# Kernel tuning notes

Measured on AMD Instinct MI355X. Metric: run time of the kernel, lower is better.

## Reference

```python
import jax, jax.numpy as jnp
import numpy as np

B, T, C, H = 2, 2048, 2048, 16
HD = C // H  # 128 head dim
ROPE_BASE = 10000.0


def setup_inputs() -> dict:
    key = jax.random.key(0)
    k0, k1, k2 = jax.random.split(key, 3)
    x = jax.random.normal(k0, (B, T, C), dtype=jnp.float32)
    W_attn = jax.random.normal(k1, (C, 3 * C), dtype=jnp.float32) * 0.02
    b_attn = jnp.zeros((3 * C,), dtype=jnp.float32)
    W_proj = jax.random.normal(k2, (C, C), dtype=jnp.float32) * 0.02
    b_proj = jnp.zeros((C,), dtype=jnp.float32)
    # freqs_cis = exp(i * t * theta_j), represented as (cos, sin), shape [T, HD//2]
    inv_freq = 1.0 / (ROPE_BASE ** (jnp.arange(0, HD, 2, dtype=jnp.float32) / HD))
    freqs = jnp.outer(jnp.arange(T, dtype=jnp.float32), inv_freq)
    return {"x": x, "W_attn": W_attn, "b_attn": b_attn, "W_proj": W_proj,
            "b_proj": b_proj, "cos": jnp.cos(freqs), "sin": jnp.sin(freqs)}


def _apply_rope(v, cos, sin):
    # v: [B, T, H, HD]; pairs (v[..., 2i], v[..., 2i+1]) rotated by angle freqs[t, i]
    vr = v.reshape(v.shape[:-1] + (-1, 2))
    x0, x1 = vr[..., 0], vr[..., 1]
    c = cos[None, :, None, :]  # [1, T, 1, HD//2]
    s = sin[None, :, None, :]
    o0 = x0 * c - x1 * s
    o1 = x0 * s + x1 * c
    return jnp.stack([o0, o1], axis=-1).reshape(v.shape)


def reference(x, W_attn, b_attn, W_proj, b_proj, cos, sin):
    Bv, Tv, Cv = x.shape
    qkv = x @ W_attn + b_attn                      # [B, T, 3C]
    q, k, v = jnp.split(qkv, 3, axis=-1)
    q = q.reshape(Bv, Tv, H, HD)
    k = k.reshape(Bv, Tv, H, HD)
    v = v.reshape(Bv, Tv, H, HD)
    q = _apply_rope(q, cos, sin)
    k = _apply_rope(k, cos, sin)
    scale = 1.0 / jnp.sqrt(jnp.float32(HD))
    att = jnp.einsum('bqhd,bkhd->bhqk', q, k) * scale
    causal = jnp.tril(jnp.ones((Tv, Tv), dtype=bool))
    att = jnp.where(causal[None, None], att, jnp.finfo(att.dtype).min)
    att = jax.nn.softmax(att, axis=-1)
    y = jnp.einsum('bhqk,bkhd->bqhd', att, v).reshape(Bv, Tv, Cv)
    return y @ W_proj + b_proj
```

## Files before the change

### kernel.cpp

```cpp
#include <hip/hip_runtime.h>

typedef unsigned short u16;
typedef __attribute__((ext_vector_type(8))) short short8;
typedef __attribute__((ext_vector_type(4))) float f32x4;

#define TSEQ 2048
#define NHEAD 16
#define HDIM 128

__device__ __forceinline__ u16 f2bf(float x) {
    unsigned u = __float_as_uint(x);
    return (u16)((u + 0x7fffu + ((u >> 16) & 1u)) >> 16);
}
__device__ __forceinline__ float b2f(u16 h) {
    return __uint_as_float(((unsigned)h) << 16);
}
__device__ __forceinline__ void async16(const void* g, void* l) {
    __builtin_amdgcn_global_load_lds((__attribute__((address_space(1))) void*)(void*)g,
                                     (__attribute__((address_space(3))) void*)l, 16, 0, 0);
}
__device__ __forceinline__ f32x4 zero4() {
    f32x4 z = {0.f, 0.f, 0.f, 0.f};
    return z;
}

template <int CTRL>
__device__ __forceinline__ float dppf(float x) {
    return __int_as_float(__builtin_amdgcn_mov_dpp(__float_as_int(x), CTRL, 0xf, 0xf, true));
}
__device__ __forceinline__ float dpp_max16(float x) {
    x = fmaxf(x, dppf<0xB1>(x));
    x = fmaxf(x, dppf<0x4E>(x));
    x = fmaxf(x, dppf<0x141>(x));
    x = fmaxf(x, dppf<0x140>(x));
    return x;
}
__device__ __forceinline__ float dpp_sum16(float x) {
    x += dppf<0xB1>(x);
    x += dppf<0x4E>(x);
    x += dppf<0x141>(x);
    x += dppf<0x140>(x);
    return x;
}

__global__ void cast_bf16(const float4* __restrict__ in, ushort4* __restrict__ out, int n4) {
    int i = blockIdx.x * 256 + threadIdx.x;
    if (i < n4) {
        float4 v = in[i];
        ushort4 o;
        o.x = f2bf(v.x); o.y = f2bf(v.y); o.z = f2bf(v.z); o.w = f2bf(v.w);
        out[i] = o;
    }
}

__global__ void transpose_cast(const float* __restrict__ in, u16* __restrict__ out, int K, int N) {
    __shared__ float tile[64][65];
    int n0 = blockIdx.x * 64, k0 = blockIdx.y * 64;
    int tx = threadIdx.x & 63, ty = threadIdx.x >> 6;
#pragma unroll
    for (int i = 0; i < 16; i++) {
        int r = ty + i * 4;
        tile[r][tx] = in[(size_t)(k0 + r) * N + n0 + tx];
    }
    __syncthreads();
#pragma unroll
    for (int i = 0; i < 16; i++) {
        int r = ty + i * 4;
        out[(size_t)(n0 + r) * K + k0 + tx] = f2bf(tile[tx][r]);
    }
}

template <int MODE>
__global__ __launch_bounds__(256) void gemm_bt(
    const u16* __restrict__ A, const u16* __restrict__ Bt, const float* __restrict__ bias,
    float* __restrict__ outf, u16* __restrict__ qb, u16* __restrict__ kb, u16* __restrict__ vT,
    const float* __restrict__ cosp, const float* __restrict__ sinp,
    int M, int N, int K) {
    __shared__ __align__(16) u16 smem[8704];
    u16* As = smem;
    u16* Bs = smem + 4096;
    const int tid = threadIdx.x;
    const int wave = tid >> 6, lane = tid & 63;
    const int low = lane & 15, quad = lane >> 4;
    const int m0 = blockIdx.y * 128, n0 = blockIdx.x * 128;
    const int wm = (wave >> 1) * 64, wn = (wave & 1) * 64;
    const int ldr = lane >> 2;
    const int ldc = (lane & 3) * 8;

    f32x4 acc[4][4];
#pragma unroll
    for (int i = 0; i < 4; i++)
#pragma unroll
        for (int j = 0; j < 4; j++) acc[i][j] = zero4();

    for (int k0 = 0; k0 < K; k0 += 32) {
#pragma unroll
        for (int c = 0; c < 2; ++c) {
            const int chunk = wave * 2 + c;
            const int row = chunk * 16 + ldr;
            async16(A + (size_t)(m0 + row) * K + k0 + ldc, As + chunk * 512);
            async16(Bt + (size_t)(n0 + row) * K + k0 + ldc, Bs + chunk * 512);
        }
        __syncthreads();
        short8 af[4], bfv[4];
#pragma unroll
        for (int i = 0; i < 4; i++) af[i] = *(const short8*)(As + (wm + i * 16 + low) * 32 + quad * 8);
#pragma unroll
        for (int j = 0; j < 4; j++) bfv[j] = *(const short8*)(Bs + (wn + j * 16 + low) * 32 + quad * 8);
#pragma unroll
        for (int i = 0; i < 4; i++)
#pragma unroll
            for (int j = 0; j < 4; j++)
                acc[i][j] = __builtin_amdgcn_mfma_f32_16x16x32_bf16(af[i], bfv[j], acc[i][j], 0, 0, 0);
        __syncthreads();
    }

    if (MODE == 1) {
#pragma unroll
        for (int j = 0; j < 4; j++) {
            const int ng = n0 + wn + j * 16 + low;
            const float bv = bias[ng];
#pragma unroll
            for (int i = 0; i < 4; i++) {
                const int rbase = m0 + wm + i * 16 + quad * 4;
#pragma unroll
                for (int r = 0; r < 4; r++)
                    outf[(size_t)(rbase + r) * N + ng] = acc[i][j][r] + bv;
            }
        }
        return;
    }
}


#define WAIT_DS()                                          \
    {                                                      \
        asm volatile("s_waitcnt lgkmcnt(0)" ::: "memory"); \
        __builtin_amdgcn_sched_barrier(0);                 \
    }
#define PRIO_MFQ(MB, NB)                \
    {                                   \
        __builtin_amdgcn_s_setprio(1);  \
        MFQ(MB, NB);                    \
        __builtin_amdgcn_s_setprio(0);  \
    }
#define BAR() __builtin_amdgcn_s_barrier();
#define VBAR(N)                                                \
    {                                                          \
        asm volatile("s_waitcnt vmcnt(" #N ")" ::: "memory");  \
        __builtin_amdgcn_s_barrier();                          \
    }

#define STAGE(GP, GROW0, LB, KT)                                                                     \
    {                                                                                                \
        const int ktc__ = ((KT) < NT ? (KT) : NT - 1);                                               \
        const u16* g0__ = (GP) + (size_t)((GROW0) + wave * 16 + grow) * (size_t)K + ktc__ * 64 +     \
                          gslot * 8;                                                                 \
        u16* l0__ = (LB) + wave * 1024;                                                              \
        async16(g0__, l0__);                                                                         \
        async16(g0__ + (size_t)8 * K, l0__ + 512);                                                   \
    }

#define LDA4(BASE, MB)                                                              \
    {                                                                               \
        _Pragma("unroll") for (int mm = 0; mm < 4; ++mm) {                          \
            a[mm][0] = *(const short8*)((BASE) + aoff0 + ((MB) + mm) * 1024);       \
            a[mm][1] = *(const short8*)((BASE) + aoff1 + ((MB) + mm) * 1024);       \
        }                                                                           \
    }
#define LDB2(BASE, NB)                                                              \
    {                                                                               \
        _Pragma("unroll") for (int nn = 0; nn < 2; ++nn) {                          \
            b[(NB) + nn][0] = *(const short8*)((BASE) + boff0 + ((NB) + nn) * 1024);\
            b[(NB) + nn][1] = *(const short8*)((BASE) + boff1 + ((NB) + nn) * 1024);\
        }                                                                           \
    }
#define MFQ(MB, NB)                                                                                   \
    {                                                                                                 \
        _Pragma("unroll") for (int mm = 0; mm < 4; ++mm) _Pragma("unroll") for (int nn = 0; nn < 2;   \
                                                                                ++nn) {               \
            acc[(MB) + mm][(NB) + nn] = __builtin_amdgcn_mfma_f32_16x16x32_bf16(                      \
                a[mm][0], b[(NB) + nn][0], acc[(MB) + mm][(NB) + nn], 0, 0, 0);                       \
            acc[(MB) + mm][(NB) + nn] = __builtin_amdgcn_mfma_f32_16x16x32_bf16(                      \
                a[mm][1], b[(NB) + nn][1], acc[(MB) + mm][(NB) + nn], 0, 0, 0);                       \
        }                                                                                             \
    }

__global__ __launch_bounds__(512, 2) void gemm256(
    const u16* __restrict__ A, const u16* __restrict__ Bt, const float* __restrict__ bias,
    u16* __restrict__ qb, u16* __restrict__ kb, u16* __restrict__ vT,
    const float* __restrict__ cosp, const float* __restrict__ sinp,
    int M, int N, int K) {
    extern __shared__ u16 sm[];
    u16* const smA0 = sm;
    u16* const smB0 = sm + 16384;
    u16* const smA1 = sm + 32768;
    u16* const smB1 = sm + 49152;

    const int tid = threadIdx.x;
    const int wave = tid >> 6, lane = tid & 63;
    const int low = lane & 15, quad = lane >> 4;
    const int wr = wave >> 2, wc = wave & 3;
    const int m0 = blockIdx.y * 256, n0 = blockIdx.x * 256;
    const int NT = K >> 6;

    const int grow = lane >> 3;
    const int gslot = (lane & 7) ^ grow;

    const int swz = low & 7;
    const int arow = (wr * 128 + low) * 64;
    const int brow = (wc * 64 + low) * 64;
    const int aoff0 = arow + ((0 + quad) ^ swz) * 8;
    const int aoff1 = arow + ((4 + quad) ^ swz) * 8;
    const int boff0 = brow + ((0 + quad) ^ swz) * 8;
    const int boff1 = brow + ((4 + quad) ^ swz) * 8;

    f32x4 acc[8][4];
#pragma unroll
    for (int i = 0; i < 8; i++)
#pragma unroll
        for (int j = 0; j < 4; j++) acc[i][j] = zero4();
    short8 a[4][2], b[4][2];

    STAGE(A, m0, smA0, 0);
    STAGE(A, m0 + 128, smA0 + 8192, 0);
    STAGE(Bt, n0, smB0, 0);
    STAGE(Bt, n0 + 128, smB0 + 8192, 0);
    STAGE(A, m0, smA1, 1);
    STAGE(A, m0 + 128, smA1 + 8192, 1);
    STAGE(Bt, n0, smB1, 1);
    STAGE(Bt, n0 + 128, smB1 + 8192, 1);
    asm volatile("s_waitcnt vmcnt(8)" ::: "memory");
    __builtin_amdgcn_s_barrier();

#pragma unroll 1
    for (int it = 0; it < (NT >> 1); ++it) {
        const int e = it * 2;
        LDA4(smA0, 0);
        LDB2(smB0, 0);
        WAIT_DS(); PRIO_MFQ(0, 0);
        LDB2(smB0, 2);
        WAIT_DS(); PRIO_MFQ(0, 2);
        LDA4(smA0, 4);
        WAIT_DS();
        BAR();
        PRIO_MFQ(4, 2);
        STAGE(A, m0, smA0, e + 2);
        STAGE(Bt, n0, smB0, e + 2);
        PRIO_MFQ(4, 0);
        VBAR(4);
        LDA4(smA1, 0);
        LDB2(smB1, 0);
        STAGE(A, m0 + 128, smA0 + 8192, e + 2);
        STAGE(Bt, n0 + 128, smB0 + 8192, e + 2);
        WAIT_DS(); PRIO_MFQ(0, 0);
        LDB2(smB1, 2);
        WAIT_DS(); PRIO_MFQ(0, 2);
        LDA4(smA1, 4);
        WAIT_DS();
        BAR();
        PRIO_MFQ(4, 2);
        STAGE(A, m0, smA1, e + 3);
        STAGE(A, m0 + 128, smA1 + 8192, e + 3);
        STAGE(Bt, n0, smB1, e + 3);
        STAGE(Bt, n0 + 128, smB1 + 8192, e + 3);
        PRIO_MFQ(4, 0);
        VBAR(8);
    }

    asm volatile("s_waitcnt vmcnt(0)" ::: "memory");
    __syncthreads();

    const int which = n0 >> 11;
    const int h0 = (n0 & 2047) >> 7;
    const int bb = m0 >> 11, t0 = m0 & 2047;
    float bvv[4];
#pragma unroll
    for (int nn = 0; nn < 4; ++nn) bvv[nn] = bias[n0 + wc * 64 + nn * 16 + low];

    if (which < 2) {
        u16* dstb = (which == 0 ? qb : kb);
        u16* epi = sm;
#pragma unroll
        for (int hh = 0; hh < 2; ++hh) {
            if ((wc >> 1) == hh) {
#pragma unroll
                for (int mm = 0; mm < 8; ++mm)
#pragma unroll
                    for (int nn = 0; nn < 4; ++nn)
#pragma unroll
                        for (int rr = 0; rr < 4; ++rr)
                            epi[(wr * 128 + mm * 16 + quad * 4 + rr) * 136 +
                                (wc & 1) * 64 + nn * 16 + low] = f2bf(acc[mm][nn][rr] + bvv[nn]);
            }
            __syncthreads();
            {
                const int row = tid >> 1, dh = (tid & 1) * 64;
                const int t = t0 + row;
                u16* dr = dstb + (((size_t)(bb * NHEAD + h0 + hh)) * TSEQ + t) * HDIM + dh;
                u16 vals[64];
#pragma unroll
                for (int qq = 0; qq < 8; ++qq)
                    *(short8*)(vals + qq * 8) = *(const short8*)(epi + row * 136 + dh + qq * 8);
                float csv[32], snv[32];
#pragma unroll
                for (int qq = 0; qq < 8; ++qq) {
                    *(float4*)(csv + qq * 4) =
                        *(const float4*)(cosp + (size_t)t * 64 + (dh >> 1) + qq * 4);
                    *(float4*)(snv + qq * 4) =
                        *(const float4*)(sinp + (size_t)t * 64 + (dh >> 1) + qq * 4);
                }
                u16 ov[64];
#pragma unroll
                for (int pp = 0; pp < 32; ++pp) {
                    float x0 = b2f(vals[2 * pp]), x1 = b2f(vals[2 * pp + 1]);
                    ov[2 * pp] = f2bf(x0 * csv[pp] - x1 * snv[pp]);
                    ov[2 * pp + 1] = f2bf(x0 * snv[pp] + x1 * csv[pp]);
                }
#pragma unroll
                for (int qq = 0; qq < 8; ++qq)
                    *(short8*)(dr + qq * 8) = *(const short8*)(ov + qq * 8);
            }
            __syncthreads();
        }
    } else {
        u16* epi = sm;
#pragma unroll
        for (int hh = 0; hh < 2; ++hh) {
            if ((wc >> 1) == hh) {
#pragma unroll
                for (int mm = 0; mm < 8; ++mm)
#pragma unroll
                    for (int nn = 0; nn < 4; ++nn)
#pragma unroll
                        for (int rr = 0; rr < 4; ++rr)
                            epi[((wc & 1) * 64 + nn * 16 + low) * 264 +
                                wr * 128 + mm * 16 + quad * 4 + rr] = f2bf(acc[mm][nn][rr] + bvv[nn]);
            }
            __syncthreads();
            {
                const int dd = tid >> 2, tc = (tid & 3) * 64;
                u16* dr = vT + ((size_t)(bb * NHEAD + h0 + hh) * HDIM + dd) * TSEQ + t0 + tc;
#pragma unroll
                for (int qq = 0; qq < 8; ++qq)
                    *(short8*)(dr + qq * 8) = *(const short8*)(epi + dd * 264 + tc + qq * 8);
            }
            __syncthreads();
        }
    }
}

__global__ __launch_bounds__(256) void flash_attn(const u16* __restrict__ qb, const u16* __restrict__ kb,
                                                  const u16* __restrict__ vT, u16* __restrict__ y) {
    __shared__ u16 Ks[64 * 128];
    __shared__ u16 Vs[128 * 64];
    __shared__ u16 Ps[4][16 * 72];
    const int tid = threadIdx.x;
    const int wave = tid >> 6, lane = tid & 63;
    const int low = lane & 15, quad = lane >> 4;
    const int bh = blockIdx.x;
    const int qt = 31 - blockIdx.y;
    const int q0 = qt * 64 + wave * 16;
    const float scale2 = 0.08838834764831845f * 1.44269504088896f;

    const u16* Qp = qb + ((size_t)bh * TSEQ + q0) * HDIM;
    short8 qf[4];
#pragma unroll
    for (int c = 0; c < 4; c++) qf[c] = *(const short8*)(Qp + (size_t)low * HDIM + c * 32 + quad * 8);

    f32x4 o[8];
#pragma unroll
    for (int d = 0; d < 8; d++) o[d] = zero4();
    float m_i[4], l_i[4];
#pragma unroll
    for (int r = 0; r < 4; r++) { m_i[r] = -1e30f; l_i[r] = 0.f; }

    const u16* Kb = kb + (size_t)bh * TSEQ * HDIM;
    const u16* Vb = vT + (size_t)bh * HDIM * TSEQ;
    u16* Pw = &Ps[wave][0];
    const int ntiles = qt + 1;

    const int krow = tid >> 4, kchunk = tid & 15;
    const int vrow = tid >> 3, vchunk = tid & 7;

    for (int kt = 0; kt < ntiles; ++kt) {
        const int kv0 = kt * 64;
#pragma unroll
        for (int j = 0; j < 4; j++) {
            const int row = j * 16 + krow;
            const int gc = kchunk ^ (row & 7);
            async16(Kb + (size_t)(kv0 + row) * HDIM + gc * 8, Ks + row * 128 + kchunk * 8);
        }
#pragma unroll
        for (int j = 0; j < 4; j++) {
            const int d = j * 32 + vrow;
            const int gc = vchunk ^ (d & 7);
            async16(Vb + (size_t)d * TSEQ + kv0 + gc * 8, Vs + d * 64 + vchunk * 8);
        }
        __syncthreads();

        f32x4 s[4];
#pragma unroll
        for (int h = 0; h < 4; h++) s[h] = zero4();
#pragma unroll
        for (int h = 0; h < 4; h++) {
            const int row = h * 16 + low;
#pragma unroll
            for (int c = 0; c < 4; c++) {
                const int cc = c * 4 + quad;
                short8 kf = *(const short8*)(Ks + row * 128 + (cc ^ (row & 7)) * 8);
                s[h] = __builtin_amdgcn_mfma_f32_16x16x32_bf16(qf[c], kf, s[h], 0, 0, 0);
            }
        }

        float alpha[4];
#pragma unroll
        for (int r = 0; r < 4; r++) {
            const int qg = q0 + quad * 4 + r;
            float sv[4];
#pragma unroll
            for (int h = 0; h < 4; h++)
                sv[h] = (kv0 + h * 16 + low <= qg) ? s[h][r] * scale2 : -1e30f;
            float mx = fmaxf(fmaxf(sv[0], sv[1]), fmaxf(sv[2], sv[3]));
            mx = dpp_max16(mx);
            float mnew = fmaxf(m_i[r], mx);
            alpha[r] = exp2f(m_i[r] - mnew);
            m_i[r] = mnew;
            float p0 = exp2f(sv[0] - mnew);
            float p1 = exp2f(sv[1] - mnew);
            float p2 = exp2f(sv[2] - mnew);
            float p3 = exp2f(sv[3] - mnew);
            float rs = (p0 + p1) + (p2 + p3);
            rs = dpp_sum16(rs);
            l_i[r] = l_i[r] * alpha[r] + rs;
            const int prow = (quad * 4 + r) * 72;
            Pw[prow + low] = f2bf(p0);
            Pw[prow + 16 + low] = f2bf(p1);
            Pw[prow + 32 + low] = f2bf(p2);
            Pw[prow + 48 + low] = f2bf(p3);
        }
        __threadfence_block();

#pragma unroll
        for (int d = 0; d < 8; ++d)
#pragma unroll
            for (int r = 0; r < 4; r++) o[d][r] *= alpha[r];

#pragma unroll
        for (int kc = 0; kc < 2; kc++) {
            short8 pf = *(const short8*)(Pw + low * 72 + kc * 32 + quad * 8);
#pragma unroll
            for (int dd = 0; dd < 8; ++dd) {
                const int vr = dd * 16 + low;
                const int cc = kc * 4 + quad;
                short8 vf = *(const short8*)(Vs + vr * 64 + (cc ^ (vr & 7)) * 8);
                o[dd] = __builtin_amdgcn_mfma_f32_16x16x32_bf16(pf, vf, o[dd], 0, 0, 0);
            }
        }
        __syncthreads();
    }

    const int b = bh >> 4, h = bh & 15;
#pragma unroll
    for (int r = 0; r < 4; r++) {
        float inv = 1.0f / l_i[r];
        size_t row = (size_t)(b * TSEQ + q0 + quad * 4 + r);
        u16* yp = y + row * 2048 + h * HDIM;
#pragma unroll
        for (int d = 0; d < 8; ++d) yp[d * 16 + low] = f2bf(o[d][r] * inv);
    }
}

extern "C" void kernel_launch(void* const* d_in, const int* in_sizes, int n_in,
                              void* d_out, int out_size, void* d_ws, size_t ws_size,
                              hipStream_t stream) {
    const float* x = (const float*)d_in[0];
    const float* Wa = (const float*)d_in[1];
    const float* ba = (const float*)d_in[2];
    const float* Wp = (const float*)d_in[3];
    const float* bp = (const float*)d_in[4];
    const float* cs = (const float*)d_in[5];
    const float* sn = (const float*)d_in[6];
    float* out = (float*)d_out;

    u16* xb = (u16*)d_ws;
    u16* Wab = xb + 8388608;
    u16* Wpb = Wab + 12582912;
    u16* qb = Wpb + 4194304;
    u16* kb = qb + 8388608;
    u16* vT = kb + 8388608;
    u16* y = xb;

    static bool attr_set = false;
    if (!attr_set) {
        hipFuncSetAttribute(reinterpret_cast<const void*>(gemm256),
                            hipFuncAttributeMaxDynamicSharedMemorySize, 131072);
        attr_set = true;
    }

    cast_bf16<<<8192, 256, 0, stream>>>((const float4*)x, (ushort4*)xb, 2097152);
    transpose_cast<<<dim3(96, 32), 256, 0, stream>>>(Wa, Wab, 2048, 6144);
    transpose_cast<<<dim3(32, 32), 256, 0, stream>>>(Wp, Wpb, 2048, 2048);
    gemm256<<<dim3(24, 16), 512, 131072, stream>>>(xb, Wab, ba, qb, kb, vT, cs, sn, 4096, 6144, 2048);
    flash_attn<<<dim3(32, 32), 256, 0, stream>>>(qb, kb, vT, y);
    gemm_bt<1><<<dim3(16, 32), 256, 0, stream>>>(y, Wpb, bp, out, nullptr, nullptr, nullptr, nullptr, nullptr, 4096, 2048, 2048);
}
```

Before: 421.3 us.

## Replace output projection GEMM with pipelined 128x256 kernel and peel QKV loop tail

Replaces the simple single-buffered output-projection GEMM with a new double-buffered, swizzled-LDS, 512-thread 128x256-tile kernel that prefetches async loads ahead of MFMA work. The QKV GEMM main loop now runs one fewer iteration and peels the last two K-steps into an epilogue, which removes the clamped redundant prefetches. It also drops the intermediate LDS waits between the MFMA groups. The intent is to hide global-load latency and raise MFMA utilization in both GEMMs. The cost is more LDS per block and reliance on the compiler inserting correct waits where the explicit ones were removed.

```diff
diff --git a/kernel.cpp b/kernel.cpp
--- a/kernel.cpp
+++ b/kernel.cpp
@@ -70,95 +70,26 @@
     }
 }
 
-template <int MODE>
-__global__ __launch_bounds__(256) void gemm_bt(
-    const u16* __restrict__ A, const u16* __restrict__ Bt, const float* __restrict__ bias,
-    float* __restrict__ outf, u16* __restrict__ qb, u16* __restrict__ kb, u16* __restrict__ vT,
-    const float* __restrict__ cosp, const float* __restrict__ sinp,
-    int M, int N, int K) {
-    __shared__ __align__(16) u16 smem[8704];
-    u16* As = smem;
-    u16* Bs = smem + 4096;
-    const int tid = threadIdx.x;
-    const int wave = tid >> 6, lane = tid & 63;
-    const int low = lane & 15, quad = lane >> 4;
-    const int m0 = blockIdx.y * 128, n0 = blockIdx.x * 128;
-    const int wm = (wave >> 1) * 64, wn = (wave & 1) * 64;
-    const int ldr = lane >> 2;
-    const int ldc = (lane & 3) * 8;
-
-    f32x4 acc[4][4];
-#pragma unroll
-    for (int i = 0; i < 4; i++)
-#pragma unroll
-        for (int j = 0; j < 4; j++) acc[i][j] = zero4();
-
-    for (int k0 = 0; k0 < K; k0 += 32) {
-#pragma unroll
-        for (int c = 0; c < 2; ++c) {
-            const int chunk = wave * 2 + c;
-            const int row = chunk * 16 + ldr;
-            async16(A + (size_t)(m0 + row) * K + k0 + ldc, As + chunk * 512);
-            async16(Bt + (size_t)(n0 + row) * K + k0 + ldc, Bs + chunk * 512);
-        }
-        __syncthreads();
-        short8 af[4], bfv[4];
-#pragma unroll
-        for (int i = 0; i < 4; i++) af[i] = *(const short8*)(As + (wm + i * 16 + low) * 32 + quad * 8);
-#pragma unroll
-        for (int j = 0; j < 4; j++) bfv[j] = *(const short8*)(Bs + (wn + j * 16 + low) * 32 + quad * 8);
-#pragma unroll
-        for (int i = 0; i < 4; i++)
-#pragma unroll
-            for (int j = 0; j < 4; j++)
-                acc[i][j] = __builtin_amdgcn_mfma_f32_16x16x32_bf16(af[i], bfv[j], acc[i][j], 0, 0, 0);
-        __syncthreads();
-    }
-
-    if (MODE == 1) {
-#pragma unroll
-        for (int j = 0; j < 4; j++) {
-            const int ng = n0 + wn + j * 16 + low;
-            const float bv = bias[ng];
-#pragma unroll
-            for (int i = 0; i < 4; i++) {
-                const int rbase = m0 + wm + i * 16 + quad * 4;
-#pragma unroll
-                for (int r = 0; r < 4; r++)
-                    outf[(size_t)(rbase + r) * N + ng] = acc[i][j][r] + bv;
-            }
-        }
-        return;
-    }
-}
-
-
 #define WAIT_DS()                                          \
     {                                                      \
         asm volatile("s_waitcnt lgkmcnt(0)" ::: "memory"); \
         __builtin_amdgcn_sched_barrier(0);                 \
     }
-#define PRIO_MFQ(MB, NB)                \
-    {                                   \
-        __builtin_amdgcn_s_setprio(1);  \
-        MFQ(MB, NB);                    \
-        __builtin_amdgcn_s_setprio(0);  \
-    }
 #define BAR() __builtin_amdgcn_s_barrier();
-#define VBAR(N)                                                \
+#define VBAR_(N)                                               \
     {                                                          \
         asm volatile("s_waitcnt vmcnt(" #N ")" ::: "memory");  \
         __builtin_amdgcn_s_barrier();                          \
     }
-
-#define STAGE(GP, GROW0, LB, KT)                                                                     \
-    {                                                                                                \
-        const int ktc__ = ((KT) < NT ? (KT) : NT - 1);                                               \
-        const u16* g0__ = (GP) + (size_t)((GROW0) + wave * 16 + grow) * (size_t)K + ktc__ * 64 +     \
-                          gslot * 8;                                                                 \
-        u16* l0__ = (LB) + wave * 1024;                                                              \
-        async16(g0__, l0__);                                                                         \
-        async16(g0__ + (size_t)8 * K, l0__ + 512);                                                   \
+#define VBAR(N) VBAR_(N)
+
+#define STAGE(GP, GROW0, LB, KT)                                                                 \
+    {                                                                                            \
+        const u16* g0__ = (GP) + (size_t)((GROW0) + wave * 16 + grow) * (size_t)K + (KT)*64 +    \
+                          gslot * 8;                                                             \
+        u16* l0__ = (LB) + wave * 1024;                                                          \
+        async16(g0__, l0__);                                                                     \
+        async16(g0__ + (size_t)8 * K, l0__ + 512);                                               \
     }
 
 #define LDA4(BASE, MB)                                                              \
@@ -184,6 +115,12 @@
             acc[(MB) + mm][(NB) + nn] = __builtin_amdgcn_mfma_f32_16x16x32_bf16(                      \
                 a[mm][1], b[(NB) + nn][1], acc[(MB) + mm][(NB) + nn], 0, 0, 0);                       \
         }                                                                                             \
+    }
+#define PRIO_MFQ(MB, NB)                \
+    {                                   \
+        __builtin_amdgcn_s_setprio(1);  \
+        MFQ(MB, NB);                    \
+        __builtin_amdgcn_s_setprio(0);  \
     }
 
 __global__ __launch_bounds__(512, 2) void gemm256(
@@ -230,17 +167,17 @@
     STAGE(A, m0 + 128, smA1 + 8192, 1);
     STAGE(Bt, n0, smB1, 1);
     STAGE(Bt, n0 + 128, smB1 + 8192, 1);
-    asm volatile("s_waitcnt vmcnt(8)" ::: "memory");
-    __builtin_amdgcn_s_barrier();
-
+    VBAR(8);
+
+    const int NI = (NT >> 1) - 1;
 #pragma unroll 1
-    for (int it = 0; it < (NT >> 1); ++it) {
+    for (int it = 0; it < NI; ++it) {
         const int e = it * 2;
         LDA4(smA0, 0);
         LDB2(smB0, 0);
-        WAIT_DS(); PRIO_MFQ(0, 0);
         LDB2(smB0, 2);
-        WAIT_DS(); PRIO_MFQ(0, 2);
+        PRIO_MFQ(0, 0);
+        PRIO_MFQ(0, 2);
         LDA4(smA0, 4);
         WAIT_DS();
         BAR();
@@ -251,11 +188,11 @@
         VBAR(4);
         LDA4(smA1, 0);
         LDB2(smB1, 0);
+        LDB2(smB1, 2);
         STAGE(A, m0 + 128, smA0 + 8192, e + 2);
         STAGE(Bt, n0 + 128, smB0 + 8192, e + 2);
-        WAIT_DS(); PRIO_MFQ(0, 0);
-        LDB2(smB1, 2);
-        WAIT_DS(); PRIO_MFQ(0, 2);
+        PRIO_MFQ(0, 0);
+        PRIO_MFQ(0, 2);
         LDA4(smA1, 4);
         WAIT_DS();
         BAR();
@@ -267,8 +204,24 @@
         PRIO_MFQ(4, 0);
         VBAR(8);
     }
-
-    asm volatile("s_waitcnt vmcnt(0)" ::: "memory");
+    LDA4(smA0, 0);
+    LDB2(smB0, 0);
+    LDB2(smB0, 2);
+    PRIO_MFQ(0, 0);
+    PRIO_MFQ(0, 2);
+    LDA4(smA0, 4);
+    PRIO_MFQ(4, 2);
+    PRIO_MFQ(4, 0);
+    VBAR(0);
+    LDA4(smA1, 0);
+    LDB2(smB1, 0);
+    LDB2(smB1, 2);
+    PRIO_MFQ(0, 0);
+    PRIO_MFQ(0, 2);
+    LDA4(smA1, 4);
+    PRIO_MFQ(4, 2);
+    PRIO_MFQ(4, 0);
+
     __syncthreads();
 
     const int which = n0 >> 11;
@@ -346,6 +299,120 @@
                     *(short8*)(dr + qq * 8) = *(const short8*)(epi + dd * 264 + tc + qq * 8);
             }
             __syncthreads();
+        }
+    }
+}
+
+#define PMFQ(NB)                                                                                      \
+    {                                                                                                 \
+        _Pragma("unroll") for (int mm = 0; mm < 4; ++mm) _Pragma("unroll") for (int nn = 0; nn < 2;   \
+                                                                                ++nn) {               \
+            acc[mm][(NB) + nn] = __builtin_amdgcn_mfma_f32_16x16x32_bf16(                             \
+                a[mm][0], b[(NB) + nn][0], acc[mm][(NB) + nn], 0, 0, 0);                              \
+            acc[mm][(NB) + nn] = __builtin_amdgcn_mfma_f32_16x16x32_bf16(                             \
+                a[mm][1], b[(NB) + nn][1], acc[mm][(NB) + nn], 0, 0, 0);                              \
+        }                                                                                             \
+    }
+#define PPRIO_MFQ(NB)                   \
+    {                                   \
+        __builtin_amdgcn_s_setprio(1);  \
+        PMFQ(NB);                       \
+        __builtin_amdgcn_s_setprio(0);  \
+    }
+
+__global__ __launch_bounds__(512, 2) void pgemm(
+    const u16* __restrict__ A, const u16* __restrict__ Bt, const float* __restrict__ bias,
+    float* __restrict__ outf, int M, int N, int K) {
+    extern __shared__ u16 sm[];
+    u16* const smA0 = sm;
+    u16* const smB0 = sm + 8192;
+    u16* const smA1 = sm + 24576;
+    u16* const smB1 = sm + 32768;
+
+    const int tid = threadIdx.x;
+    const int wave = tid >> 6, lane = tid & 63;
+    const int low = lane & 15, quad = lane >> 4;
+    const int wr = wave >> 2, wc = wave & 3;
+    const int m0 = blockIdx.y * 128, n0 = blockIdx.x * 256;
+    const int NT = K >> 6;
+
+    const int grow = lane >> 3;
+    const int gslot = (lane & 7) ^ grow;
+
+    const int swz = low & 7;
+    const int arow = (wr * 64 + low) * 64;
+    const int brow = (wc * 64 + low) * 64;
+    const int aoff0 = arow + ((0 + quad) ^ swz) * 8;
+    const int aoff1 = arow + ((4 + quad) ^ swz) * 8;
+    const int boff0 = brow + ((0 + quad) ^ swz) * 8;
+    const int boff1 = brow + ((4 + quad) ^ swz) * 8;
+
+    f32x4 acc[4][4];
+#pragma unroll
+    for (int i = 0; i < 4; i++)
+#pragma unroll
+        for (int j = 0; j < 4; j++) acc[i][j] = zero4();
+    short8 a[4][2], b[4][2];
+
+    STAGE(A, m0, smA0, 0);
+    STAGE(Bt, n0, smB0, 0);
+    STAGE(Bt, n0 + 128, smB0 + 8192, 0);
+    STAGE(A, m0, smA1, 1);
+    STAGE(Bt, n0, smB1, 1);
+    STAGE(Bt, n0 + 128, smB1 + 8192, 1);
+    VBAR(6);
+
+    const int NI = (NT >> 1) - 1;
+#pragma unroll 1
+    for (int it = 0; it < NI; ++it) {
+        const int e = it * 2;
+        LDA4(smA0, 0);
+        LDB2(smB0, 0);
+        LDB2(smB0, 2);
+        PPRIO_MFQ(0);
+        WAIT_DS();
+        BAR();
+        STAGE(A, m0, smA0, e + 2);
+        STAGE(Bt, n0, smB0, e + 2);
+        STAGE(Bt, n0 + 128, smB0 + 8192, e + 2);
+        PPRIO_MFQ(2);
+        VBAR(6);
+        LDA4(smA1, 0);
+        LDB2(smB1, 0);
+        LDB2(smB1, 2);
+        PPRIO_MFQ(0);
+        WAIT_DS();
+        BAR();
+        STAGE(A, m0, smA1, e + 3);
+        STAGE(Bt, n0, smB1, e + 3);
+        STAGE(Bt, n0 + 128, smB1 + 8192, e + 3);
+        PPRIO_MFQ(2);
+        VBAR(6);
+    }
+    LDA4(smA0, 0);
+    LDB2(smB0, 0);
+    LDB2(smB0, 2);
+    PPRIO_MFQ(0);
+    PPRIO_MFQ(2);
+    VBAR(0);
+    LDA4(smA1, 0);
+    LDB2(smB1, 0);
+    LDB2(smB1, 2);
+    PPRIO_MFQ(0);
+    PPRIO_MFQ(2);
+
+    float bvv[4];
+#pragma unroll
+    for (int nn = 0; nn < 4; ++nn) bvv[nn] = bias[n0 + wc * 64 + nn * 16 + low];
+#pragma unroll
+    for (int mm = 0; mm < 4; ++mm) {
+        const int rbase = m0 + wr * 64 + mm * 16 + quad * 4;
+#pragma unroll
+        for (int nn = 0; nn < 4; ++nn) {
+            const int col = n0 + wc * 64 + nn * 16 + low;
+#pragma unroll
+            for (int r = 0; r < 4; ++r)
+                outf[(size_t)(rbase + r) * N + col] = acc[mm][nn][r] + bvv[nn];
         }
     }
 }
@@ -495,6 +562,8 @@
     if (!attr_set) {
         hipFuncSetAttribute(reinterpret_cast<const void*>(gemm256),
                             hipFuncAttributeMaxDynamicSharedMemorySize, 131072);
+        hipFuncSetAttribute(reinterpret_cast<const void*>(pgemm),
+                            hipFuncAttributeMaxDynamicSharedMemorySize, 98304);
         attr_set = true;
     }
 
@@ -503,5 +572,5 @@
     transpose_cast<<<dim3(32, 32), 256, 0, stream>>>(Wp, Wpb, 2048, 2048);
     gemm256<<<dim3(24, 16), 512, 131072, stream>>>(xb, Wab, ba, qb, kb, vT, cs, sn, 4096, 6144, 2048);
     flash_attn<<<dim3(32, 32), 256, 0, stream>>>(qb, kb, vT, y);
-    gemm_bt<1><<<dim3(16, 32), 256, 0, stream>>>(y, Wpb, bp, out, nullptr, nullptr, nullptr, nullptr, nullptr, 4096, 2048, 2048);
-}
+    pgemm<<<dim3(8, 32), 512, 98304, stream>>>(y, Wpb, bp, out, 4096, 2048, 2048);
+}
```

Result: faster. 395.4 us (-6.1%).
